# Kernel optimization log

Hardware: AMD Instinct MI355X
Metric: run time of the kernel (lower is better)

Reference implementation:

```python
import jax, jax.numpy as jnp
import numpy as np

N = 50000   # total nodes
D = 128     # feature dim
E = 800000  # edges (avg degree 16)
G = 100     # graphs (500 nodes each)


def setup_inputs() -> dict:
    key = jax.random.key(0)
    ks = jax.random.split(key, 9)
    s = 1.0 / np.sqrt(D)
    X = jax.random.normal(ks[0], (N, D), jnp.float32)
    src = jax.random.randint(ks[1], (E,), 0, N)
    dst = jax.random.randint(ks[2], (E,), 0, N)
    edge_index = jnp.stack([src, dst])  # [2, E]
    edge_weight = jax.random.uniform(ks[3], (E,), jnp.float32)
    # 100 graphs of 500 nodes each (graph_sizes = [500]*100)
    segment_ids = jnp.repeat(jnp.arange(G), N // G)
    return {
        "X": X,
        "edge_weight": edge_weight,
        "W1": jax.random.normal(ks[4], (D, D), jnp.float32) * s,
        "b1": jnp.zeros((D,), jnp.float32),
        "W2": jax.random.normal(ks[5], (D, D), jnp.float32) * s,
        "b2": jnp.zeros((D,), jnp.float32),
        "Wf": jax.random.normal(ks[6], (D, 1), jnp.float32) * s,
        "bf": jnp.zeros((1,), jnp.float32),
        "edge_index": edge_index,
        "segment_ids": segment_ids,
    }


def gcn_conv(X, edge_index, edge_weight, W, b):
    # h_v = sum_{(u->v)} w_e * (X @ W)[u] + b   (sparse A @ XW)
    h = X @ W                                   # [N, d_out]
    msgs = h[edge_index[0]] * edge_weight[:, None]  # [E, d_out]
    agg = jax.ops.segment_sum(msgs, edge_index[1], num_segments=N)
    return agg + b


def reference(X, edge_weight, W1, b1, W2, b2, Wf, bf, edge_index, segment_ids):
    # layer stack: conv -> relu -> dropout(eval=identity)
    h = jax.nn.relu(gcn_conv(X, edge_index, edge_weight, W1, b1))
    h = jax.nn.relu(gcn_conv(h, edge_index, edge_weight, W2, b2))
    out = jax.nn.sigmoid(gcn_conv(h, edge_index, edge_weight, Wf, bf))  # [N, 1]
    # fused per-graph mean readout (replaces split(graph_sizes) python loop)
    sums = jax.ops.segment_sum(out.sum(axis=1), segment_ids, num_segments=G)
    counts = jax.ops.segment_sum(jnp.ones((N,), out.dtype), segment_ids, num_segments=G)
    return sums / (counts * out.shape[1])  # [G]
```

## Files before the change

kernel.cpp:

```cpp
#include <hip/hip_runtime.h>
#include <hip/hip_fp16.h>

#define N_NODES 50000
#define DIM 128
#define NEDGE 800000
#define NGRAPH 100
#define NPG 500
#define NBUCKET 250
#define NPB 200
#define BCAP 4096
#define CHUNK 2048
#define EPT (CHUNK / 256)

typedef _Float16 f16x8 __attribute__((ext_vector_type(8)));
typedef float f32x4 __attribute__((ext_vector_type(4)));
typedef float f32x2 __attribute__((ext_vector_type(2)));

__device__ inline float wgt(unsigned p) {
    return __half2float(__ushort_as_half((unsigned short)(p & 0xffffu)));
}
__device__ inline void accrow(uint2 q, float w, float* acc) {
    f32x2 f;
    f = __builtin_amdgcn_cvt_pk_f32_fp8((int)q.x, false); acc[0] = fmaf(w, f[0], acc[0]); acc[1] = fmaf(w, f[1], acc[1]);
    f = __builtin_amdgcn_cvt_pk_f32_fp8((int)q.x, true);  acc[2] = fmaf(w, f[0], acc[2]); acc[3] = fmaf(w, f[1], acc[3]);
    f = __builtin_amdgcn_cvt_pk_f32_fp8((int)q.y, false); acc[4] = fmaf(w, f[0], acc[4]); acc[5] = fmaf(w, f[1], acc[5]);
    f = __builtin_amdgcn_cvt_pk_f32_fp8((int)q.y, true);  acc[6] = fmaf(w, f[0], acc[6]); acc[7] = fmaf(w, f[1], acc[7]);
}
__device__ inline unsigned pack_fp8x4(float a, float b, float c, float d) {
    int v = __builtin_amdgcn_cvt_pk_fp8_f32(a, b, 0, false);
    v = __builtin_amdgcn_cvt_pk_fp8_f32(c, d, v, true);
    return (unsigned)v;
}

__global__ void prep(const float* __restrict__ W1, const float* __restrict__ W2,
                     _Float16* __restrict__ fragW1, _Float16* __restrict__ fragW2,
                     int* __restrict__ gCur) {
    const int b = blockIdx.x;
    if (b == 128) {
        int t = threadIdx.x;
        if (t < NBUCKET) gCur[t] = t * BCAP;
        return;
    }
    const float* W = (b < 64) ? W1 : W2;
    _Float16* F = (b < 64) ? fragW1 : fragW2;
    int idx = (b & 63) * 256 + threadIdx.x;
    int j = idx & 7, l = (idx >> 3) & 63, kt = (idx >> 9) & 3, nt = idx >> 11;
    int k = kt * 32 + ((l >> 4) << 3) + j;
    int col = (nt << 4) + (l & 15);
    F[idx] = (_Float16)W[k * DIM + col];
}

__global__ void bucket_scatter(const int* __restrict__ src, const int* __restrict__ dst,
                               const float* __restrict__ w, int* __restrict__ gCur,
                               uint2* __restrict__ stage, int E) {
    __shared__ int hist[NBUCKET];
    __shared__ int base[NBUCKET];
    for (int i = threadIdx.x; i < NBUCKET; i += 256) hist[i] = 0;
    __syncthreads();
    const int e0 = blockIdx.x * CHUNK;
    int myDst[EPT];
#pragma unroll
    for (int j = 0; j < EPT; ++j) {
        int e = e0 + j * 256 + threadIdx.x;
        int d = (e < E) ? dst[e] : -1;
        myDst[j] = d;
        if (d >= 0) atomicAdd(&hist[d / NPB], 1);
    }
    __syncthreads();
    for (int i = threadIdx.x; i < NBUCKET; i += 256)
        base[i] = atomicAdd(&gCur[i], hist[i]);
    __syncthreads();
#pragma unroll
    for (int j = 0; j < EPT; ++j) {
        int d = myDst[j];
        if (d >= 0) {
            int e = e0 + j * 256 + threadIdx.x;
            int b = d / NPB;
            int p = atomicAdd(&base[b], 1);
            unsigned short wh = __half_as_ushort(__float2half_rn(w[e]));
            stage[p] = make_uint2(((unsigned)src[e] << 16) | (unsigned)wh,
                                  (unsigned)(d - b * NPB));
        }
    }
}

__device__ inline f16x8 load_afrag_f32(const float* a) {
    float4 u0 = *(const float4*)a;
    float4 u1 = *(const float4*)(a + 4);
    f16x8 r;
    r[0] = (_Float16)u0.x; r[1] = (_Float16)u0.y; r[2] = (_Float16)u0.z; r[3] = (_Float16)u0.w;
    r[4] = (_Float16)u1.x; r[5] = (_Float16)u1.y; r[6] = (_Float16)u1.z; r[7] = (_Float16)u1.w;
    return r;
}

__device__ inline void gemm_tile_f32(const float* __restrict__ A, const _Float16* fragW,
                                     unsigned char* __restrict__ C, int blk, int tid) {
    const int lane = tid & 63;
    const int wid = tid >> 6;
    const int row0 = blk * 128 + wid * 16;
    if (row0 >= N_NODES) return;
    const int arow = row0 + (lane & 15);
    const int koff = (lane >> 4) << 3;
    f32x4 acc[8] = {};
#pragma unroll
    for (int kt = 0; kt < 4; ++kt) {
        f16x8 a = load_afrag_f32(A + (size_t)arow * DIM + kt * 32 + koff);
#pragma unroll
        for (int nt = 0; nt < 8; ++nt) {
            f16x8 b = *(const f16x8*)&fragW[(((nt << 2) | kt) << 9) | (lane << 3)];
            acc[nt] = __builtin_amdgcn_mfma_f32_16x16x32_f16(a, b, acc[nt], 0, 0, 0);
        }
    }
    const int crow = row0 + ((lane >> 4) << 2);
    const int ccol = lane & 15;
#pragma unroll
    for (int nt = 0; nt < 8; ++nt) {
#pragma unroll
        for (int r = 0; r < 4; ++r) {
            int v8 = __builtin_amdgcn_cvt_pk_fp8_f32(acc[nt][r], acc[nt][r], 0, false);
            C[(size_t)(crow + r) * DIM + (nt << 4) + ccol] = (unsigned char)(v8 & 0xff);
        }
    }
}

#define MFMA_BLK ((N_NODES + 127) / 128)
__global__ __launch_bounds__(512) void gemm1_build(
        const float* __restrict__ A, const _Float16* __restrict__ fragWg,
        unsigned char* __restrict__ C, const int* __restrict__ gCur,
        const uint2* __restrict__ stage, unsigned int* __restrict__ pack,
        int2* __restrict__ range) {
    __shared__ __align__(16) _Float16 fragW[16384];
    __shared__ int lhist[NPB];
    __shared__ int lincl[256];
    __shared__ int lcur[NPB];
    const int tid = threadIdx.x;
    if (blockIdx.x < MFMA_BLK) {
        for (int i = tid; i < 2048; i += 512)
            ((uint4*)fragW)[i] = ((const uint4*)fragWg)[i];
        __syncthreads();
        gemm_tile_f32(A, fragW, C, blockIdx.x, tid);
        return;
    }
    const int b = blockIdx.x - MFMA_BLK;
    const int t = tid;
    const int cnt = gCur[b] - b * BCAP;
    for (int i = t; i < NPB; i += 512) lhist[i] = 0;
    __syncthreads();
    unsigned myX[BCAP / 512];
    int myLd[BCAP / 512];
#pragma unroll
    for (int j = 0; j < BCAP / 512; ++j) {
        int i = j * 512 + t;
        if (i < cnt) {
            uint2 r = stage[b * BCAP + i];
            myX[j] = r.x;
            myLd[j] = (int)r.y;
            atomicAdd(&lhist[r.y], 1);
        } else {
            myLd[j] = -1;
        }
    }
    __syncthreads();
    int h = (t < NPB) ? lhist[t] : 0;
    if (t < 256) lincl[t] = h;
    __syncthreads();
    for (int off = 1; off < 256; off <<= 1) {
        int v = (t >= off && t < 256) ? lincl[t - off] : 0;
        __syncthreads();
        if (t < 256) lincl[t] += v;
        __syncthreads();
    }
    if (t < NPB) lcur[t] = lincl[t] - h;
    __syncthreads();
#pragma unroll
    for (int j = 0; j < BCAP / 512; ++j) {
        if (myLd[j] >= 0) {
            int p = atomicAdd(&lcur[myLd[j]], 1);
            pack[b * BCAP + p] = myX[j];
        }
    }
    if (t < NPB) {
        int v = b * NPB + t;
        range[v] = make_int2(b * BCAP + lincl[t] - h, b * BCAP + lincl[t]);
    }
}

__global__ __launch_bounds__(256) void gather_gemm2(
        const unsigned char* __restrict__ msg, const unsigned int* __restrict__ pack,
        const int2* __restrict__ range, const float* __restrict__ bias,
        const _Float16* __restrict__ fragW2, unsigned char* __restrict__ C) {
    __shared__ __align__(16) char hT[16 * 256];
    const int t = threadIdx.x;
    const int grpL = t >> 4;
    const int lane16 = t & 15;
    const int tile = blockIdx.x;
    {
        const int grp = tile * 16 + grpL;
        int2 r = range[grp];
        int beg = r.x, end = r.y;
        float acc[8] = {};
        int i = beg;
        for (; i + 7 < end; i += 8) {
            unsigned p[8];
            uint2 q[8];
#pragma unroll
            for (int j = 0; j < 8; ++j) p[j] = pack[i + j];
#pragma unroll
            for (int j = 0; j < 8; ++j)
                q[j] = ((const uint2*)(msg + (size_t)(p[j] >> 16) * DIM))[lane16];
#pragma unroll
            for (int j = 0; j < 8; ++j) accrow(q[j], wgt(p[j]), acc);
        }
        for (; i + 3 < end; i += 4) {
            unsigned p0 = pack[i], p1 = pack[i + 1], p2 = pack[i + 2], p3 = pack[i + 3];
            uint2 q0 = ((const uint2*)(msg + (size_t)(p0 >> 16) * DIM))[lane16];
            uint2 q1 = ((const uint2*)(msg + (size_t)(p1 >> 16) * DIM))[lane16];
            uint2 q2 = ((const uint2*)(msg + (size_t)(p2 >> 16) * DIM))[lane16];
            uint2 q3 = ((const uint2*)(msg + (size_t)(p3 >> 16) * DIM))[lane16];
            accrow(q0, wgt(p0), acc);
            accrow(q1, wgt(p1), acc);
            accrow(q2, wgt(p2), acc);
            accrow(q3, wgt(p3), acc);
        }
        for (; i < end; ++i) {
            unsigned p = pack[i];
            uint2 q = ((const uint2*)(msg + (size_t)(p >> 16) * DIM))[lane16];
            accrow(q, wgt(p), acc);
        }
        float4 b0 = ((const float4*)bias)[2 * lane16];
        float4 b1 = ((const float4*)bias)[2 * lane16 + 1];
        union { __half2 h[4]; uint4 u; } o;
        o.h[0] = __floats2half2_rn(fmaxf(acc[0] + b0.x, 0.f), fmaxf(acc[1] + b0.y, 0.f));
        o.h[1] = __floats2half2_rn(fmaxf(acc[2] + b0.z, 0.f), fmaxf(acc[3] + b0.w, 0.f));
        o.h[2] = __floats2half2_rn(fmaxf(acc[4] + b1.x, 0.f), fmaxf(acc[5] + b1.y, 0.f));
        o.h[3] = __floats2half2_rn(fmaxf(acc[6] + b1.z, 0.f), fmaxf(acc[7] + b1.w, 0.f));
        int boff = (grpL << 8) | (lane16 << 4);
        boff ^= (grpL & 7) << 4;
        *(uint4*)(hT + boff) = o.u;
    }
    __syncthreads();
    const int lane = t & 63;
    const int wid = t >> 6;
    const int arowL = lane & 15;
    const int koff = (lane >> 4) << 3;
    f32x4 acc2[2] = {};
#pragma unroll
    for (int kt = 0; kt < 4; ++kt) {
        int boff = (arowL << 8) | ((kt * 32 + koff) << 1);
        boff ^= (arowL & 7) << 4;
        f16x8 a = *(const f16x8*)(hT + boff);
#pragma unroll
        for (int n = 0; n < 2; ++n) {
            int nt = wid * 2 + n;
            f16x8 b = *(const f16x8*)&fragW2[(((nt << 2) | kt) << 9) | (lane << 3)];
            acc2[n] = __builtin_amdgcn_mfma_f32_16x16x32_f16(a, b, acc2[n], 0, 0, 0);
        }
    }
    const int crow = tile * 16 + ((lane >> 4) << 2);
    const int ccol = lane & 15;
#pragma unroll
    for (int n = 0; n < 2; ++n) {
#pragma unroll
        for (int r = 0; r < 4; ++r) {
            int v8 = __builtin_amdgcn_cvt_pk_fp8_f32(acc2[n][r], acc2[n][r], 0, false);
            C[(size_t)(crow + r) * DIM + ((wid * 2 + n) << 4) + ccol] = (unsigned char)(v8 & 0xff);
        }
    }
}

__global__ void gather_wf(const unsigned char* __restrict__ msg,
                          const unsigned int* __restrict__ pack,
                          const int2* __restrict__ range, const float* __restrict__ bias,
                          const float* __restrict__ wf, float* __restrict__ outS) {
    int gid = blockIdx.x * blockDim.x + threadIdx.x;
    int grp = gid >> 4, lane = gid & 15;
    if (grp >= N_NODES) return;
    int2 r = range[grp];
    int beg = r.x, end = r.y;
    float acc[8] = {};
    int i = beg;
    for (; i + 7 < end; i += 8) {
        unsigned p[8];
        uint2 q[8];
#pragma unroll
        for (int j = 0; j < 8; ++j) p[j] = pack[i + j];
#pragma unroll
        for (int j = 0; j < 8; ++j)
            q[j] = ((const uint2*)(msg + (size_t)(p[j] >> 16) * DIM))[lane];
#pragma unroll
        for (int j = 0; j < 8; ++j) accrow(q[j], wgt(p[j]), acc);
    }
    for (; i + 3 < end; i += 4) {
        unsigned p0 = pack[i], p1 = pack[i + 1], p2 = pack[i + 2], p3 = pack[i + 3];
        uint2 q0 = ((const uint2*)(msg + (size_t)(p0 >> 16) * DIM))[lane];
        uint2 q1 = ((const uint2*)(msg + (size_t)(p1 >> 16) * DIM))[lane];
        uint2 q2 = ((const uint2*)(msg + (size_t)(p2 >> 16) * DIM))[lane];
        uint2 q3 = ((const uint2*)(msg + (size_t)(p3 >> 16) * DIM))[lane];
        accrow(q0, wgt(p0), acc);
        accrow(q1, wgt(p1), acc);
        accrow(q2, wgt(p2), acc);
        accrow(q3, wgt(p3), acc);
    }
    for (; i < end; ++i) {
        unsigned p = pack[i];
        uint2 q = ((const uint2*)(msg + (size_t)(p >> 16) * DIM))[lane];
        accrow(q, wgt(p), acc);
    }
    float4 b0 = ((const float4*)bias)[2 * lane];
    float4 b1 = ((const float4*)bias)[2 * lane + 1];
    float4 f0 = ((const float4*)wf)[2 * lane];
    float4 f1 = ((const float4*)wf)[2 * lane + 1];
    float d = fmaxf(acc[0] + b0.x, 0.f) * f0.x + fmaxf(acc[1] + b0.y, 0.f) * f0.y
            + fmaxf(acc[2] + b0.z, 0.f) * f0.z + fmaxf(acc[3] + b0.w, 0.f) * f0.w
            + fmaxf(acc[4] + b1.x, 0.f) * f1.x + fmaxf(acc[5] + b1.y, 0.f) * f1.y
            + fmaxf(acc[6] + b1.z, 0.f) * f1.z + fmaxf(acc[7] + b1.w, 0.f) * f1.w;
#pragma unroll
    for (int off = 8; off; off >>= 1) d += __shfl_down(d, off, 16);
    if (lane == 0) outS[grp] = d;
}

__global__ void final_readout(const float* __restrict__ s, const unsigned int* __restrict__ pack,
                              const int2* __restrict__ range, const float* __restrict__ bfp,
                              float* __restrict__ out) {
    __shared__ float red[256];
    int g = blockIdx.x;
    float bf = bfp[0];
    float sum = 0.f;
    for (int n = threadIdx.x; n < NPG; n += blockDim.x) {
        int v = g * NPG + n;
        int2 r = range[v];
        float a = 0.f;
        for (int i = r.x; i < r.y; ++i) {
            unsigned int p = pack[i];
            a += wgt(p) * s[p >> 16];
        }
        a += bf;
        sum += 1.f / (1.f + expf(-a));
    }
    red[threadIdx.x] = sum;
    __syncthreads();
    for (int t = 128; t > 0; t >>= 1) {
        if (threadIdx.x < t) red[threadIdx.x] += red[threadIdx.x + t];
        __syncthreads();
    }
    if (threadIdx.x == 0) out[g] = red[0] / (float)NPG;
}

extern "C" void kernel_launch(void* const* d_in, const int* in_sizes, int n_in,
                              void* d_out, int out_size, void* d_ws, size_t ws_size,
                              hipStream_t stream) {
    const float* X  = (const float*)d_in[0];
    const float* ew = (const float*)d_in[1];
    const float* W1 = (const float*)d_in[2];
    const float* b1 = (const float*)d_in[3];
    const float* W2 = (const float*)d_in[4];
    const float* b2 = (const float*)d_in[5];
    const float* Wf = (const float*)d_in[6];
    const float* bf = (const float*)d_in[7];
    const int* ei   = (const int*)d_in[8];
    const int* src  = ei;
    const int* dst  = ei + NEDGE;

    float* out = (float*)d_out;

    char* ws = (char*)d_ws;
    size_t off = 0;
    unsigned char* bufA = (unsigned char*)(ws + off); off += (size_t)N_NODES * DIM;
    unsigned char* bufB = (unsigned char*)(ws + off); off += (size_t)N_NODES * DIM;
    uint2* stage = (uint2*)(ws + off);  off += (size_t)NBUCKET * BCAP * 8;
    unsigned int* pack = (unsigned int*)(ws + off); off += (size_t)NBUCKET * BCAP * 4;
    int2* range = (int2*)(ws + off);    off += (size_t)N_NODES * 8;
    int* gCur   = (int*)(ws + off);     off += (size_t)256 * 4;
    _Float16* fragW1 = (_Float16*)(ws + off); off += (size_t)16384 * 2;
    _Float16* fragW2 = (_Float16*)(ws + off); off += (size_t)16384 * 2;
    float* s_node = (float*)(ws + off); off += (size_t)N_NODES * 4;

    const int TB = 256;
    const int SCAT_BLK = (NEDGE + CHUNK - 1) / CHUNK;
    const int TILE_BLK = N_NODES / 16;
    const int GATHER_BLK = (N_NODES * 16 + TB - 1) / TB;

    prep<<<129, TB, 0, stream>>>(W1, W2, fragW1, fragW2, gCur);
    bucket_scatter<<<SCAT_BLK, TB, 0, stream>>>(src, dst, ew, gCur, stage, NEDGE);
    gemm1_build<<<MFMA_BLK + NBUCKET, 512, 0, stream>>>(X, fragW1, bufA, gCur,
                                                        stage, pack, range);
    gather_gemm2<<<TILE_BLK, TB, 0, stream>>>(bufA, pack, range, b1, fragW2, bufB);
    gather_wf<<<GATHER_BLK, TB, 0, stream>>>(bufB, pack, range, b2, Wf, s_node);
    final_readout<<<NGRAPH, TB, 0, stream>>>(s_node, pack, range, bf, out);
}
```

Measured before the change: 99.02 us.

## Gather 16-byte row slices with 8 lanes per node and widen gemm2 tiles

The gather kernels now use 8 lanes per destination node, each loading a uint4 (16 fp8 values) per edge instead of a uint2 with 16 lanes, so there are fewer, wider memory requests and twice as many nodes per block. gather_gemm2 now handles 32 rows per block, with each wave computing 4 MFMA column tiles, and a tail guard is added. The scatter CHUNK doubles, which halves the number of scatter blocks. In exchange, each thread holds more registers (16 accumulators and 8 uint4 loads in flight), which may lower occupancy and latency hiding.

```diff
diff --git a/kernel.cpp b/kernel.cpp
--- a/kernel.cpp
+++ b/kernel.cpp
@@ -9,7 +9,7 @@
 #define NBUCKET 250
 #define NPB 200
 #define BCAP 4096
-#define CHUNK 2048
+#define CHUNK 4096
 #define EPT (CHUNK / 256)
 
 typedef _Float16 f16x8 __attribute__((ext_vector_type(8)));
@@ -19,17 +19,16 @@
 __device__ inline float wgt(unsigned p) {
     return __half2float(__ushort_as_half((unsigned short)(p & 0xffffu)));
 }
-__device__ inline void accrow(uint2 q, float w, float* acc) {
+__device__ inline void accrow16(uint4 q, float w, float* acc) {
     f32x2 f;
-    f = __builtin_amdgcn_cvt_pk_f32_fp8((int)q.x, false); acc[0] = fmaf(w, f[0], acc[0]); acc[1] = fmaf(w, f[1], acc[1]);
-    f = __builtin_amdgcn_cvt_pk_f32_fp8((int)q.x, true);  acc[2] = fmaf(w, f[0], acc[2]); acc[3] = fmaf(w, f[1], acc[3]);
-    f = __builtin_amdgcn_cvt_pk_f32_fp8((int)q.y, false); acc[4] = fmaf(w, f[0], acc[4]); acc[5] = fmaf(w, f[1], acc[5]);
-    f = __builtin_amdgcn_cvt_pk_f32_fp8((int)q.y, true);  acc[6] = fmaf(w, f[0], acc[6]); acc[7] = fmaf(w, f[1], acc[7]);
-}
-__device__ inline unsigned pack_fp8x4(float a, float b, float c, float d) {
-    int v = __builtin_amdgcn_cvt_pk_fp8_f32(a, b, 0, false);
-    v = __builtin_amdgcn_cvt_pk_fp8_f32(c, d, v, true);
-    return (unsigned)v;
+    f = __builtin_amdgcn_cvt_pk_f32_fp8((int)q.x, false); acc[0]  = fmaf(w, f[0], acc[0]);  acc[1]  = fmaf(w, f[1], acc[1]);
+    f = __builtin_amdgcn_cvt_pk_f32_fp8((int)q.x, true);  acc[2]  = fmaf(w, f[0], acc[2]);  acc[3]  = fmaf(w, f[1], acc[3]);
+    f = __builtin_amdgcn_cvt_pk_f32_fp8((int)q.y, false); acc[4]  = fmaf(w, f[0], acc[4]);  acc[5]  = fmaf(w, f[1], acc[5]);
+    f = __builtin_amdgcn_cvt_pk_f32_fp8((int)q.y, true);  acc[6]  = fmaf(w, f[0], acc[6]);  acc[7]  = fmaf(w, f[1], acc[7]);
+    f = __builtin_amdgcn_cvt_pk_f32_fp8((int)q.z, false); acc[8]  = fmaf(w, f[0], acc[8]);  acc[9]  = fmaf(w, f[1], acc[9]);
+    f = __builtin_amdgcn_cvt_pk_f32_fp8((int)q.z, true);  acc[10] = fmaf(w, f[0], acc[10]); acc[11] = fmaf(w, f[1], acc[11]);
+    f = __builtin_amdgcn_cvt_pk_f32_fp8((int)q.w, false); acc[12] = fmaf(w, f[0], acc[12]); acc[13] = fmaf(w, f[1], acc[13]);
+    f = __builtin_amdgcn_cvt_pk_f32_fp8((int)q.w, true);  acc[14] = fmaf(w, f[0], acc[14]); acc[15] = fmaf(w, f[1], acc[15]);
 }
 
 __global__ void prep(const float* __restrict__ W1, const float* __restrict__ W2,
@@ -185,85 +184,102 @@
     }
 }
 
+__device__ inline void gather_core(const unsigned char* __restrict__ msg,
+                                   const unsigned int* __restrict__ pack,
+                                   int beg, int end, int lane8, float* acc) {
+    int i = beg;
+    for (; i + 7 < end; i += 8) {
+        unsigned p[8];
+        uint4 q[8];
+#pragma unroll
+        for (int j = 0; j < 8; ++j) p[j] = pack[i + j];
+#pragma unroll
+        for (int j = 0; j < 8; ++j)
+            q[j] = ((const uint4*)(msg + (size_t)(p[j] >> 16) * DIM))[lane8];
+#pragma unroll
+        for (int j = 0; j < 8; ++j) accrow16(q[j], wgt(p[j]), acc);
+    }
+    for (; i + 3 < end; i += 4) {
+        unsigned p0 = pack[i], p1 = pack[i + 1], p2 = pack[i + 2], p3 = pack[i + 3];
+        uint4 q0 = ((const uint4*)(msg + (size_t)(p0 >> 16) * DIM))[lane8];
+        uint4 q1 = ((const uint4*)(msg + (size_t)(p1 >> 16) * DIM))[lane8];
+        uint4 q2 = ((const uint4*)(msg + (size_t)(p2 >> 16) * DIM))[lane8];
+        uint4 q3 = ((const uint4*)(msg + (size_t)(p3 >> 16) * DIM))[lane8];
+        accrow16(q0, wgt(p0), acc);
+        accrow16(q1, wgt(p1), acc);
+        accrow16(q2, wgt(p2), acc);
+        accrow16(q3, wgt(p3), acc);
+    }
+    for (; i < end; ++i) {
+        unsigned p = pack[i];
+        uint4 q = ((const uint4*)(msg + (size_t)(p >> 16) * DIM))[lane8];
+        accrow16(q, wgt(p), acc);
+    }
+}
+
 __global__ __launch_bounds__(256) void gather_gemm2(
         const unsigned char* __restrict__ msg, const unsigned int* __restrict__ pack,
         const int2* __restrict__ range, const float* __restrict__ bias,
         const _Float16* __restrict__ fragW2, unsigned char* __restrict__ C) {
-    __shared__ __align__(16) char hT[16 * 256];
+    __shared__ __align__(16) char hT[32 * 256];
     const int t = threadIdx.x;
-    const int grpL = t >> 4;
-    const int lane16 = t & 15;
+    const int grpL = t >> 3;
+    const int lane8 = t & 7;
     const int tile = blockIdx.x;
-    {
-        const int grp = tile * 16 + grpL;
+    const int grp = tile * 32 + grpL;
+    if (grp < N_NODES) {
         int2 r = range[grp];
-        int beg = r.x, end = r.y;
-        float acc[8] = {};
-        int i = beg;
-        for (; i + 7 < end; i += 8) {
-            unsigned p[8];
-            uint2 q[8];
-#pragma unroll
-            for (int j = 0; j < 8; ++j) p[j] = pack[i + j];
-#pragma unroll
-            for (int j = 0; j < 8; ++j)
-                q[j] = ((const uint2*)(msg + (size_t)(p[j] >> 16) * DIM))[lane16];
-#pragma unroll
-            for (int j = 0; j < 8; ++j) accrow(q[j], wgt(p[j]), acc);
-        }
-        for (; i + 3 < end; i += 4) {
-            unsigned p0 = pack[i], p1 = pack[i + 1], p2 = pack[i + 2], p3 = pack[i + 3];
-            uint2 q0 = ((const uint2*)(msg + (size_t)(p0 >> 16) * DIM))[lane16];
-            uint2 q1 = ((const uint2*)(msg + (size_t)(p1 >> 16) * DIM))[lane16];
-            uint2 q2 = ((const uint2*)(msg + (size_t)(p2 >> 16) * DIM))[lane16];
-            uint2 q3 = ((const uint2*)(msg + (size_t)(p3 >> 16) * DIM))[lane16];
-            accrow(q0, wgt(p0), acc);
-            accrow(q1, wgt(p1), acc);
-            accrow(q2, wgt(p2), acc);
-            accrow(q3, wgt(p3), acc);
-        }
-        for (; i < end; ++i) {
-            unsigned p = pack[i];
-            uint2 q = ((const uint2*)(msg + (size_t)(p >> 16) * DIM))[lane16];
-            accrow(q, wgt(p), acc);
-        }
-        float4 b0 = ((const float4*)bias)[2 * lane16];
-        float4 b1 = ((const float4*)bias)[2 * lane16 + 1];
-        union { __half2 h[4]; uint4 u; } o;
-        o.h[0] = __floats2half2_rn(fmaxf(acc[0] + b0.x, 0.f), fmaxf(acc[1] + b0.y, 0.f));
-        o.h[1] = __floats2half2_rn(fmaxf(acc[2] + b0.z, 0.f), fmaxf(acc[3] + b0.w, 0.f));
-        o.h[2] = __floats2half2_rn(fmaxf(acc[4] + b1.x, 0.f), fmaxf(acc[5] + b1.y, 0.f));
-        o.h[3] = __floats2half2_rn(fmaxf(acc[6] + b1.z, 0.f), fmaxf(acc[7] + b1.w, 0.f));
-        int boff = (grpL << 8) | (lane16 << 4);
-        boff ^= (grpL & 7) << 4;
-        *(uint4*)(hT + boff) = o.u;
+        float acc[16] = {};
+        gather_core(msg, pack, r.x, r.y, lane8, acc);
+        float4 b0 = ((const float4*)bias)[4 * lane8 + 0];
+        float4 b1 = ((const float4*)bias)[4 * lane8 + 1];
+        float4 b2 = ((const float4*)bias)[4 * lane8 + 2];
+        float4 b3 = ((const float4*)bias)[4 * lane8 + 3];
+        union { __half2 h[8]; uint4 u[2]; } o;
+        o.h[0] = __floats2half2_rn(fmaxf(acc[0]  + b0.x, 0.f), fmaxf(acc[1]  + b0.y, 0.f));
+        o.h[1] = __floats2half2_rn(fmaxf(acc[2]  + b0.z, 0.f), fmaxf(acc[3]  + b0.w, 0.f));
+        o.h[2] = __floats2half2_rn(fmaxf(acc[4]  + b1.x, 0.f), fmaxf(acc[5]  + b1.y, 0.f));
+        o.h[3] = __floats2half2_rn(fmaxf(acc[6]  + b1.z, 0.f), fmaxf(acc[7]  + b1.w, 0.f));
+        o.h[4] = __floats2half2_rn(fmaxf(acc[8]  + b2.x, 0.f), fmaxf(acc[9]  + b2.y, 0.f));
+        o.h[5] = __floats2half2_rn(fmaxf(acc[10] + b2.z, 0.f), fmaxf(acc[11] + b2.w, 0.f));
+        o.h[6] = __floats2half2_rn(fmaxf(acc[12] + b3.x, 0.f), fmaxf(acc[13] + b3.y, 0.f));
+        o.h[7] = __floats2half2_rn(fmaxf(acc[14] + b3.z, 0.f), fmaxf(acc[15] + b3.w, 0.f));
+        int base = (grpL << 8) | (lane8 << 5);
+        int m = (grpL & 7) << 4;
+        *(uint4*)(hT + ((base) ^ m)) = o.u[0];
+        *(uint4*)(hT + ((base + 16) ^ m)) = o.u[1];
     }
     __syncthreads();
     const int lane = t & 63;
     const int wid = t >> 6;
-    const int arowL = lane & 15;
+    const int rt = wid >> 1;
+    const int ntBase = (wid & 1) << 2;
+    const int arow = rt * 16 + (lane & 15);
     const int koff = (lane >> 4) << 3;
-    f32x4 acc2[2] = {};
+    f32x4 acc2[4] = {};
 #pragma unroll
     for (int kt = 0; kt < 4; ++kt) {
-        int boff = (arowL << 8) | ((kt * 32 + koff) << 1);
-        boff ^= (arowL & 7) << 4;
+        int boff = (arow << 8) | (((kt << 5) + koff) << 1);
+        boff ^= (arow & 7) << 4;
         f16x8 a = *(const f16x8*)(hT + boff);
 #pragma unroll
-        for (int n = 0; n < 2; ++n) {
-            int nt = wid * 2 + n;
+        for (int n = 0; n < 4; ++n) {
+            int nt = ntBase + n;
             f16x8 b = *(const f16x8*)&fragW2[(((nt << 2) | kt) << 9) | (lane << 3)];
             acc2[n] = __builtin_amdgcn_mfma_f32_16x16x32_f16(a, b, acc2[n], 0, 0, 0);
         }
     }
-    const int crow = tile * 16 + ((lane >> 4) << 2);
-    const int ccol = lane & 15;
-#pragma unroll
-    for (int n = 0; n < 2; ++n) {
-#pragma unroll
-        for (int r = 0; r < 4; ++r) {
-            int v8 = __builtin_amdgcn_cvt_pk_fp8_f32(acc2[n][r], acc2[n][r], 0, false);
-            C[(size_t)(crow + r) * DIM + ((wid * 2 + n) << 4) + ccol] = (unsigned char)(v8 & 0xff);
+    const int rowBase = tile * 32 + rt * 16;
+    if (rowBase < N_NODES) {
+        const int crow = rowBase + ((lane >> 4) << 2);
+        const int ccol = lane & 15;
+#pragma unroll
+        for (int n = 0; n < 4; ++n) {
+#pragma unroll
+            for (int r = 0; r < 4; ++r) {
+                int v8 = __builtin_amdgcn_cvt_pk_fp8_f32(acc2[n][r], acc2[n][r], 0, false);
+                C[(size_t)(crow + r) * DIM + ((ntBase + n) << 4) + ccol] = (unsigned char)(v8 & 0xff);
+            }
         }
     }
 }
@@ -273,50 +289,30 @@
                           const int2* __restrict__ range, const float* __restrict__ bias,
                           const float* __restrict__ wf, float* __restrict__ outS) {
     int gid = blockIdx.x * blockDim.x + threadIdx.x;
-    int grp = gid >> 4, lane = gid & 15;
+    int grp = gid >> 3, lane8 = gid & 7;
     if (grp >= N_NODES) return;
     int2 r = range[grp];
-    int beg = r.x, end = r.y;
-    float acc[8] = {};
-    int i = beg;
-    for (; i + 7 < end; i += 8) {
-        unsigned p[8];
-        uint2 q[8];
-#pragma unroll
-        for (int j = 0; j < 8; ++j) p[j] = pack[i + j];
-#pragma unroll
-        for (int j = 0; j < 8; ++j)
-            q[j] = ((const uint2*)(msg + (size_t)(p[j] >> 16) * DIM))[lane];
-#pragma unroll
-        for (int j = 0; j < 8; ++j) accrow(q[j], wgt(p[j]), acc);
-    }
-    for (; i + 3 < end; i += 4) {
-        unsigned p0 = pack[i], p1 = pack[i + 1], p2 = pack[i + 2], p3 = pack[i + 3];
-        uint2 q0 = ((const uint2*)(msg + (size_t)(p0 >> 16) * DIM))[lane];
-        uint2 q1 = ((const uint2*)(msg + (size_t)(p1 >> 16) * DIM))[lane];
-        uint2 q2 = ((const uint2*)(msg + (size_t)(p2 >> 16) * DIM))[lane];
-        uint2 q3 = ((const uint2*)(msg + (size_t)(p3 >> 16) * DIM))[lane];
-        accrow(q0, wgt(p0), acc);
-        accrow(q1, wgt(p1), acc);
-        accrow(q2, wgt(p2), acc);
-        accrow(q3, wgt(p3), acc);
-    }
-    for (; i < end; ++i) {
-        unsigned p = pack[i];
-        uint2 q = ((const uint2*)(msg + (size_t)(p >> 16) * DIM))[lane];
-        accrow(q, wgt(p), acc);
-    }
-    float4 b0 = ((const float4*)bias)[2 * lane];
-    float4 b1 = ((const float4*)bias)[2 * lane + 1];
-    float4 f0 = ((const float4*)wf)[2 * lane];
-    float4 f1 = ((const float4*)wf)[2 * lane + 1];
-    float d = fmaxf(acc[0] + b0.x, 0.f) * f0.x + fmaxf(acc[1] + b0.y, 0.f) * f0.y
-            + fmaxf(acc[2] + b0.z, 0.f) * f0.z + fmaxf(acc[3] + b0.w, 0.f) * f0.w
-            + fmaxf(acc[4] + b1.x, 0.f) * f1.x + fmaxf(acc[5] + b1.y, 0.f) * f1.y
-            + fmaxf(acc[6] + b1.z, 0.f) * f1.z + fmaxf(acc[7] + b1.w, 0.f) * f1.w;
-#pragma unroll
-    for (int off = 8; off; off >>= 1) d += __shfl_down(d, off, 16);
-    if (lane == 0) outS[grp] = d;
+    float acc[16] = {};
+    gather_core(msg, pack, r.x, r.y, lane8, acc);
+    float4 b0 = ((const float4*)bias)[4 * lane8 + 0];
+    float4 b1 = ((const float4*)bias)[4 * lane8 + 1];
+    float4 b2 = ((const float4*)bias)[4 * lane8 + 2];
+    float4 b3 = ((const float4*)bias)[4 * lane8 + 3];
+    float4 f0 = ((const float4*)wf)[4 * lane8 + 0];
+    float4 f1 = ((const float4*)wf)[4 * lane8 + 1];
+    float4 f2 = ((const float4*)wf)[4 * lane8 + 2];
+    float4 f3 = ((const float4*)wf)[4 * lane8 + 3];
+    float d = fmaxf(acc[0]  + b0.x, 0.f) * f0.x + fmaxf(acc[1]  + b0.y, 0.f) * f0.y
+            + fmaxf(acc[2]  + b0.z, 0.f) * f0.z + fmaxf(acc[3]  + b0.w, 0.f) * f0.w
+            + fmaxf(acc[4]  + b1.x, 0.f) * f1.x + fmaxf(acc[5]  + b1.y, 0.f) * f1.y
+            + fmaxf(acc[6]  + b1.z, 0.f) * f1.z + fmaxf(acc[7]  + b1.w, 0.f) * f1.w
+            + fmaxf(acc[8]  + b2.x, 0.f) * f2.x + fmaxf(acc[9]  + b2.y, 0.f) * f2.y
+            + fmaxf(acc[10] + b2.z, 0.f) * f2.z + fmaxf(acc[11] + b2.w, 0.f) * f2.w
+            + fmaxf(acc[12] + b3.x, 0.f) * f3.x + fmaxf(acc[13] + b3.y, 0.f) * f3.y
+            + fmaxf(acc[14] + b3.z, 0.f) * f3.z + fmaxf(acc[15] + b3.w, 0.f) * f3.w;
+#pragma unroll
+    for (int off = 4; off; off >>= 1) d += __shfl_down(d, off, 8);
+    if (lane8 == 0) outS[grp] = d;
 }
 
 __global__ void final_readout(const float* __restrict__ s, const unsigned int* __restrict__ pack,
@@ -377,8 +373,8 @@
 
     const int TB = 256;
     const int SCAT_BLK = (NEDGE + CHUNK - 1) / CHUNK;
-    const int TILE_BLK = N_NODES / 16;
-    const int GATHER_BLK = (N_NODES * 16 + TB - 1) / TB;
+    const int TILE_BLK = (N_NODES + 31) / 32;
+    const int GATHER_BLK = (N_NODES * 8 + TB - 1) / TB;
 
     prep<<<129, TB, 0, stream>>>(W1, W2, fragW1, fragW2, gCur);
     bucket_scatter<<<SCAT_BLK, TB, 0, stream>>>(src, dst, ew, gCur, stage, NEDGE);
```

Result: no change. 100.9 us (+1.9%).
